# Performance work log

Hardware: AMD Instinct MI355X
Metric: run time of the kernel (lower is better)

Reference implementation:

```python
import jax, jax.numpy as jnp
import numpy as np

B, C, H, W = 4, 256, 64, 64
CH = C // 2  # inner channels


def setup_inputs() -> dict:
    key = jax.random.key(0)
    ks = jax.random.split(key, 9)
    s = 1.0 / np.sqrt(C)
    so = 1.0 / np.sqrt(CH)
    return {
        "x": jax.random.normal(ks[0], (B, C, H, W), dtype=jnp.float32),
        "teta_w": jax.random.uniform(ks[1], (CH, C), jnp.float32, -s, s),
        "teta_b": jax.random.uniform(ks[2], (CH,), jnp.float32, -s, s),
        "fi_w": jax.random.uniform(ks[3], (CH, C), jnp.float32, -s, s),
        "fi_b": jax.random.uniform(ks[4], (CH,), jnp.float32, -s, s),
        "gi_w": jax.random.uniform(ks[5], (CH, C), jnp.float32, -s, s),
        "gi_b": jax.random.uniform(ks[6], (CH,), jnp.float32, -s, s),
        "out_w": jax.random.uniform(ks[7], (C, CH), jnp.float32, -so, so),
        "out_b": jax.random.uniform(ks[8], (C,), jnp.float32, -so, so),
    }


def _conv1x1(x, w, b):
    # x: (B, Cin, H, W), w: (Cout, Cin) -> (B, Cout, H, W)
    return jnp.einsum('bchw,oc->bohw', x, w) + b[None, :, None, None]


def reference(x, teta_w, teta_b, fi_w, fi_b, gi_w, gi_b, out_w, out_b):
    b, c, h, w = x.shape
    n = h * w
    ch = teta_w.shape[0]
    # NOTE: original uses .view (reshape), NOT transpose, to get (B, N, Ch)
    x1 = _conv1x1(x, teta_w, teta_b).reshape(b, ch, n).reshape(b, n, ch)
    x2 = _conv1x1(x, fi_w, fi_b).reshape(b, ch, n)            # (B, Ch, N)
    x3 = _conv1x1(x, gi_w, gi_b).reshape(b, ch, n).reshape(b, n, ch)
    # softmax over dim=1 (rows), as in the original
    attn = jax.nn.softmax(jnp.matmul(x1, x2), axis=1)          # (B, N, N)
    y = jnp.matmul(attn, x3)                                   # (B, N, Ch)
    y = jnp.swapaxes(y, 1, 2).reshape(b, ch, h, w)
    return x + _conv1x1(y, out_w, out_b)
```

## Files before the change

kernel.cpp:

```cpp
#include <hip/hip_runtime.h>
#include <hip/hip_bf16.h>

#define BB 4
#define CC 256
#define CHH 128
#define NN 4096
#define KSHIFT 12.0f

typedef __attribute__((ext_vector_type(8))) short bf16x8;
typedef __attribute__((ext_vector_type(4))) float f32x4;

__device__ __forceinline__ float to_f(float v) { return v; }
__device__ __forceinline__ float to_f(__hip_bfloat16 v) { return __bfloat162float(v); }
__device__ __forceinline__ void st_f(float* p, float v) { *p = v; }
__device__ __forceinline__ void st_f(__hip_bfloat16* p, float v) { *p = __float2bfloat16(v); }
__device__ __forceinline__ unsigned short f2bf(float f) {
    __hip_bfloat16 h = __float2bfloat16(f);
    unsigned short u;
    __builtin_memcpy(&u, &h, 2);
    return u;
}
__device__ __forceinline__ bf16x8 ldb8(const unsigned short* p) { return *(const bf16x8*)p; }

__device__ __forceinline__ void gload_lds16(const unsigned short* g, unsigned short* l) {
    __builtin_amdgcn_global_load_lds(
        (const __attribute__((address_space(1))) unsigned int*)g,
        (__attribute__((address_space(3))) unsigned int*)l, 16, 0, 0);
}

__global__ void detect_kernel(const void* __restrict__ tb, int* __restrict__ flag) {
    if (threadIdx.x == 0) {
        const __hip_bfloat16* p = (const __hip_bfloat16*)tb;
        int big = 0, zeros = 0;
        for (int i = 0; i < 128; ++i) {
            float v = __bfloat162float(p[i]);
            if (!(fabsf(v) <= 0.5f)) big = 1;
            if ((i & 1) == 0 && v == 0.0f) zeros++;
        }
        *flag = (big || zeros >= 32) ? 1 : 0;
    }
}

template <typename T>
__device__ __forceinline__ void prep_body(const T* tw, const T* fw, const T* gw, const T* ow,
                                          const T* tb2, const T* fb, const T* gb, const T* ob,
                                          unsigned short* Wb, unsigned short* OWb,
                                          float* Bf, float* OBf) {
    int idx = blockIdx.x * 256 + threadIdx.x;
    if (idx < 98304) {
        int cv = idx >> 15, rem = idx & 32767;
        const T* src = cv == 0 ? tw : (cv == 1 ? fw : gw);
        Wb[idx] = f2bf(to_f(src[rem]));
    } else if (idx < 131072) {
        OWb[idx - 98304] = f2bf(to_f(ow[idx - 98304]));
    } else if (idx < 131456) {
        int r = idx - 131072;
        int cv = r >> 7, j = r & 127;
        const T* src = cv == 0 ? tb2 : (cv == 1 ? fb : gb);
        Bf[r] = to_f(src[j]);
    } else if (idx < 131712) {
        OBf[idx - 131456] = to_f(ob[idx - 131456]);
    }
}

__global__ void prep_kernel(const void* tw, const void* fw, const void* gw, const void* ow,
                            const void* tb2, const void* fb, const void* gb, const void* ob,
                            const int* __restrict__ flag,
                            unsigned short* Wb, unsigned short* OWb, float* Bf, float* OBf) {
    if (*flag)
        prep_body<float>((const float*)tw, (const float*)fw, (const float*)gw, (const float*)ow,
                         (const float*)tb2, (const float*)fb, (const float*)gb, (const float*)ob,
                         Wb, OWb, Bf, OBf);
    else
        prep_body<__hip_bfloat16>((const __hip_bfloat16*)tw, (const __hip_bfloat16*)fw,
                                  (const __hip_bfloat16*)gw, (const __hip_bfloat16*)ow,
                                  (const __hip_bfloat16*)tb2, (const __hip_bfloat16*)fb,
                                  (const __hip_bfloat16*)gb, (const __hip_bfloat16*)ob,
                                  Wb, OWb, Bf, OBf);
}

template <typename T>
__device__ __forceinline__ void xtrans_body(const T* __restrict__ x, unsigned short* __restrict__ xt) {
    int b = blockIdx.z;
    const T* in = x + (size_t)b * CC * NN;
    unsigned short* out = xt + (size_t)b * NN * CC;
    int p0 = blockIdx.x * 64, c0 = blockIdx.y * 64;
    __shared__ unsigned short t[64][68];
    int flat = threadIdx.x;
#pragma unroll
    for (int tt = 0; tt < 16; ++tt) {
        int id = flat + tt * 256;
        int rr = id >> 6, cc = id & 63;
        t[cc][rr] = f2bf(to_f(in[(size_t)(c0 + rr) * NN + p0 + cc]));
    }
    __syncthreads();
#pragma unroll
    for (int tt = 0; tt < 16; ++tt) {
        int id = flat + tt * 256;
        int pp = id >> 6, jj = id & 63;
        out[(size_t)(p0 + pp) * CC + c0 + jj] = t[pp][jj];
    }
}

__launch_bounds__(256)
__global__ void xtrans_kernel(const void* x, const int* __restrict__ flag,
                              unsigned short* __restrict__ xt) {
    if (*flag) xtrans_body<float>((const float*)x, xt);
    else       xtrans_body<__hip_bfloat16>((const __hip_bfloat16*)x, xt);
}

__launch_bounds__(256)
__global__ void conv3_mfma_kernel(const unsigned short* __restrict__ xt,
                                  const unsigned short* __restrict__ Wb,
                                  const float* __restrict__ Bf,
                                  unsigned short* __restrict__ T1b,
                                  unsigned short* __restrict__ T2t,
                                  unsigned short* __restrict__ T3b) {
    int b = blockIdx.y;
    int p0 = blockIdx.x * 16;
    int flat = threadIdx.x;
    int w = flat >> 6, lane = flat & 63, m = lane & 15, quad = lane >> 4;
    const unsigned short* xrow = xt + ((size_t)b * NN + p0 + m) * CC;
    bf16x8 xf[8];
#pragma unroll
    for (int kc = 0; kc < 8; ++kc)
        xf[kc] = ldb8(&xrow[kc * 32 + quad * 8]);
    unsigned short* t1  = T1b + (size_t)b * CHH * NN;
    unsigned short* t2t = T2t + (size_t)b * CHH * NN;
    unsigned short* t3  = T3b + (size_t)b * CHH * NN;
#pragma unroll
    for (int q = 0; q < 6; ++q) {
        int t = w * 6 + q;
        int cv = t >> 3, ot = t & 7;
        int o0 = ot * 16;
        const unsigned short* wrow = Wb + ((size_t)cv * CHH + o0 + m) * CC;
        f32x4 acc = {0.f, 0.f, 0.f, 0.f};
#pragma unroll
        for (int kc = 0; kc < 8; ++kc) {
            bf16x8 wf = ldb8(&wrow[kc * 32 + quad * 8]);
            acc = __builtin_amdgcn_mfma_f32_16x16x32_bf16(wf, xf[kc], acc, 0, 0, 0);
        }
        unsigned short hv[4];
#pragma unroll
        for (int r = 0; r < 4; ++r)
            hv[r] = f2bf(acc[r] + Bf[cv * CHH + o0 + quad * 4 + r]);
        if (cv == 1) {
            unsigned int lo = (unsigned int)hv[0] | ((unsigned int)hv[1] << 16);
            unsigned int hi = (unsigned int)hv[2] | ((unsigned int)hv[3] << 16);
            int src = (lane & 3) * 16 + (lane >> 2);
            unsigned int tlo = (unsigned int)__shfl((int)lo, src, 64);
            unsigned int thi = (unsigned int)__shfl((int)hi, src, 64);
            unsigned int* dst = (unsigned int*)&t2t[(size_t)(p0 + (lane >> 2)) * CHH +
                                                    o0 + (lane & 3) * 4];
            dst[0] = tlo;
            dst[1] = thi;
        } else {
            unsigned short* outp = (cv == 0) ? t1 : t3;
#pragma unroll
            for (int r = 0; r < 4; ++r)
                outp[(size_t)(o0 + quad * 4 + r) * NN + p0 + m] = hv[r];
        }
    }
}

__launch_bounds__(256)
__global__ void transpose_kernel(const unsigned short* __restrict__ in,
                                 unsigned short* __restrict__ out, int R, int C) {
    int bz = blockIdx.z;
    in  += (size_t)bz * R * C;
    out += (size_t)bz * R * C;
    int c0 = blockIdx.x * 64, r0 = blockIdx.y * 64;
    __shared__ unsigned short t[64][68];
    int flat = threadIdx.x;
#pragma unroll
    for (int tt = 0; tt < 16; ++tt) {
        int id = flat + tt * 256;
        int r = id >> 6, c = id & 63;
        t[c][r] = in[(size_t)(r0 + r) * C + c0 + c];
    }
    __syncthreads();
#pragma unroll
    for (int tt = 0; tt < 16; ++tt) {
        int id = flat + tt * 256;
        int c = id >> 6, r = id & 63;
        out[(size_t)(c0 + c) * R + r0 + r] = t[c][r];
    }
}

__launch_bounds__(256)
__global__ void stats_mfma_kernel(const unsigned short* __restrict__ T1b,
                                  const unsigned short* __restrict__ T2t,
                                  float* __restrict__ Lpart) {
    int blk = blockIdx.x;
    int b = (blk & 7) >> 1;
    int rest = (blk >> 3) * 2 + (blk & 1);
    int strip = rest >> 3, iq = rest & 7;
    int ibase = iq * 512;
    int flat = threadIdx.x;
    int w = flat >> 6, lane = flat & 63, m = lane & 15, quad = lane >> 4;
    const unsigned short* A  = T1b + (size_t)b * CHH * NN;
    const unsigned short* Bt = T2t + (size_t)b * CHH * NN;
    __shared__ unsigned short th[64 * 128];

    int u0w = strip * 128 + w * 32;
    bf16x8 bfr[2][4];
#pragma unroll
    for (int g = 0; g < 2; ++g)
#pragma unroll
        for (int kc = 0; kc < 4; ++kc)
            bfr[g][kc] = ldb8(&Bt[(size_t)(u0w + g * 16 + m) * CHH + kc * 32 + quad * 8]);

    float csum[2] = {0.f, 0.f};
    for (int t = 0; t < 8; ++t) {
        int i0t = ibase + t * 64;
        __syncthreads();
#pragma unroll
        for (int i = 0; i < 4; ++i) {
            int sl = i * 256 + flat;
            int r = sl >> 4, ch = sl & 15;
            int c = ch ^ (r & 7);
            gload_lds16(&A[(size_t)(i0t + r) * CHH + c * 8], &th[sl * 8]);
        }
        __syncthreads();
#pragma unroll
        for (int s = 0; s < 4; ++s) {
            int irow = s * 16 + m;
            bf16x8 af[4];
#pragma unroll
            for (int kc = 0; kc < 4; ++kc) {
                int ch = (kc * 4 + quad) ^ (irow & 7);
                af[kc] = *(const bf16x8*)&th[irow * 128 + ch * 8];
            }
#pragma unroll
            for (int g = 0; g < 2; ++g) {
                f32x4 acc = {0.f, 0.f, 0.f, 0.f};
#pragma unroll
                for (int kc = 0; kc < 4; ++kc)
                    acc = __builtin_amdgcn_mfma_f32_16x16x32_bf16(af[kc], bfr[g][kc], acc, 0, 0, 0);
#pragma unroll
                for (int r = 0; r < 4; ++r)
                    csum[g] += __expf(acc[r] - KSHIFT);
            }
        }
    }
#pragma unroll
    for (int g = 0; g < 2; ++g) {
        csum[g] += __shfl_xor(csum[g], 16, 64);
        csum[g] += __shfl_xor(csum[g], 32, 64);
        if (lane < 16)
            Lpart[((size_t)iq * BB + b) * NN + u0w + g * 16 + m] = csum[g];
    }
}

__launch_bounds__(256)
__global__ void attn_mfma_kernel(const unsigned short* __restrict__ T1b,
                                 const unsigned short* __restrict__ T2t,
                                 const unsigned short* __restrict__ X3t,
                                 const float* __restrict__ Lpart,
                                 unsigned short* __restrict__ Yp0,
                                 unsigned short* __restrict__ Yp1,
                                 unsigned short* __restrict__ Yp2,
                                 unsigned short* __restrict__ Yp3) {
    int blk = blockIdx.x;
    int b = (blk & 7) >> 1;
    int rest = (blk >> 3) * 2 + (blk & 1);
    int it = rest >> 2, uc = rest & 3;
    int i0 = it * 128;
    unsigned short* Yp = uc == 0 ? Yp0 : (uc == 1 ? Yp1 : (uc == 2 ? Yp2 : Yp3));
    int flat = threadIdx.x;
    int w = flat >> 6, lane = flat & 63, m = lane & 15, quad = lane >> 4;
    const unsigned short* A  = T1b + (size_t)b * CHH * NN;
    const unsigned short* Bt = T2t + (size_t)b * CHH * NN;
    const unsigned short* X3 = X3t + (size_t)b * CHH * NN;

    __shared__ unsigned short bt[64 * 128];
    __shared__ unsigned short x3[128 * 64];
    __shared__ unsigned short pT[4][2][16][40];
    __shared__ float llh[1024];

    int ubeg = uc * 1024;
#pragma unroll
    for (int k = 0; k < 4; ++k) {
        int idx = k * 256 + flat;
        int u = ubeg + idx;
        float s = 0.f;
#pragma unroll
        for (int c = 0; c < 8; ++c)
            s += Lpart[((size_t)c * BB + b) * NN + u];
        llh[idx] = logf(s) + KSHIFT;
    }

    int iw = i0 + w * 32;
    bf16x8 ath[2][4];
#pragma unroll
    for (int g = 0; g < 2; ++g)
#pragma unroll
        for (int kc = 0; kc < 4; ++kc)
            ath[g][kc] = ldb8(&A[(size_t)(iw + g * 16 + m) * CHH + kc * 32 + quad * 8]);
    f32x4 yacc[2][8];
#pragma unroll
    for (int g = 0; g < 2; ++g)
#pragma unroll
        for (int js = 0; js < 8; ++js) yacc[g][js] = (f32x4){0.f, 0.f, 0.f, 0.f};

    for (int u0 = ubeg; u0 < ubeg + 1024; u0 += 64) {
        __syncthreads();
#pragma unroll
        for (int i = 0; i < 4; ++i) {
            int sl = i * 256 + flat;
            int u = sl >> 4, ch = sl & 15;
            int c = ch ^ (u & 7);
            gload_lds16(&Bt[(size_t)(u0 + u) * CHH + c * 8], &bt[sl * 8]);
        }
#pragma unroll
        for (int i = 0; i < 4; ++i) {
            int sl = i * 256 + flat;
            int j = sl >> 3, ch = sl & 7;
            int c = ch ^ (j & 7);
            gload_lds16(&X3[(size_t)j * NN + u0 + c * 8], &x3[sl * 8]);
        }
        __syncthreads();
#pragma unroll
        for (int h = 0; h < 2; ++h) {
#pragma unroll
            for (int su = 0; su < 2; ++su) {
                int u = h * 32 + su * 16 + m;
                f32x4 a0 = {0.f, 0.f, 0.f, 0.f}, a1 = {0.f, 0.f, 0.f, 0.f};
#pragma unroll
                for (int kc = 0; kc < 4; ++kc) {
                    int ch = (kc * 4 + quad) ^ (u & 7);
                    bf16x8 bf = *(const bf16x8*)&bt[u * 128 + ch * 8];
                    a0 = __builtin_amdgcn_mfma_f32_16x16x32_bf16(ath[0][kc], bf, a0, 0, 0, 0);
                    a1 = __builtin_amdgcn_mfma_f32_16x16x32_bf16(ath[1][kc], bf, a1, 0, 0, 0);
                }
                float ll = llh[u0 - ubeg + u];
#pragma unroll
                for (int r = 0; r < 4; ++r) {
                    pT[w][0][quad * 4 + r][su * 16 + m] = f2bf(__expf(a0[r] - ll));
                    pT[w][1][quad * 4 + r][su * 16 + m] = f2bf(__expf(a1[r] - ll));
                }
            }
            bf16x8 pa0 = *(const bf16x8*)&pT[w][0][m][quad * 8];
            bf16x8 pa1 = *(const bf16x8*)&pT[w][1][m][quad * 8];
#pragma unroll
            for (int js = 0; js < 8; ++js) {
                int j = js * 16 + m;
                int ch = (h * 4 + quad) ^ (j & 7);
                bf16x8 xb = *(const bf16x8*)&x3[j * 64 + ch * 8];
                yacc[0][js] = __builtin_amdgcn_mfma_f32_16x16x32_bf16(pa0, xb, yacc[0][js], 0, 0, 0);
                yacc[1][js] = __builtin_amdgcn_mfma_f32_16x16x32_bf16(pa1, xb, yacc[1][js], 0, 0, 0);
            }
        }
    }
#pragma unroll
    for (int g = 0; g < 2; ++g)
#pragma unroll
        for (int js = 0; js < 8; ++js)
#pragma unroll
            for (int r = 0; r < 4; ++r)
                Yp[((size_t)b * NN + iw + g * 16 + quad * 4 + r) * CHH + js * 16 + m] =
                    f2bf(yacc[g][js][r]);
}

template <typename T>
__device__ __forceinline__ void outconv_body(const T* __restrict__ x,
                                             const unsigned short* __restrict__ Yp0,
                                             const unsigned short* __restrict__ Yp1,
                                             const unsigned short* __restrict__ Yp2,
                                             const unsigned short* __restrict__ Yp3,
                                             const unsigned short* __restrict__ OWb,
                                             const float* __restrict__ OBf,
                                             T* __restrict__ out) {
    int b = blockIdx.y;
    int p0 = blockIdx.x * 16;
    int flat = threadIdx.x;
    int w = flat >> 6, lane = flat & 63, m = lane & 15, quad = lane >> 4;
    size_t yoff = ((size_t)b * NN + p0 + m) * CHH;
    const unsigned short* yrows[4] = {Yp0 + yoff, Yp1 + yoff, Yp2 + yoff, Yp3 + yoff};
    bf16x8 yf[4][4];
#pragma unroll
    for (int pz = 0; pz < 4; ++pz)
#pragma unroll
        for (int kc = 0; kc < 4; ++kc)
            yf[pz][kc] = ldb8(&yrows[pz][kc * 32 + quad * 8]);
#pragma unroll
    for (int q = 0; q < 4; ++q) {
        int o0 = (w * 4 + q) * 16;
        const unsigned short* wrow = OWb + (size_t)(o0 + m) * CHH;
        f32x4 acc = {0.f, 0.f, 0.f, 0.f};
#pragma unroll
        for (int kc = 0; kc < 4; ++kc) {
            bf16x8 aw = ldb8(&wrow[kc * 32 + quad * 8]);
#pragma unroll
            for (int pz = 0; pz < 4; ++pz)
                acc = __builtin_amdgcn_mfma_f32_16x16x32_bf16(aw, yf[pz][kc], acc, 0, 0, 0);
        }
#pragma unroll
        for (int r = 0; r < 4; ++r) {
            int co = o0 + quad * 4 + r;
            size_t oi = ((size_t)b * CC + co) * NN + p0 + m;
            st_f(&out[oi], acc[r] + OBf[co] + to_f(x[oi]));
        }
    }
}

__launch_bounds__(256)
__global__ void outconv_mfma_kernel(const void* x,
                                    const unsigned short* __restrict__ Yp0,
                                    const unsigned short* __restrict__ Yp1,
                                    const unsigned short* __restrict__ Yp2,
                                    const unsigned short* __restrict__ Yp3,
                                    const unsigned short* __restrict__ OWb,
                                    const float* __restrict__ OBf,
                                    const int* __restrict__ flag, void* out) {
    if (*flag)
        outconv_body<float>((const float*)x, Yp0, Yp1, Yp2, Yp3, OWb, OBf, (float*)out);
    else
        outconv_body<__hip_bfloat16>((const __hip_bfloat16*)x, Yp0, Yp1, Yp2, Yp3, OWb, OBf,
                                     (__hip_bfloat16*)out);
}

extern "C" void kernel_launch(void* const* d_in, const int* in_sizes, int n_in,
                              void* d_out, int out_size, void* d_ws, size_t ws_size,
                              hipStream_t stream) {
    const void* x  = d_in[0];
    const void* tw = d_in[1];
    const void* tb = d_in[2];
    const void* fw = d_in[3];
    const void* fb = d_in[4];
    const void* gw = d_in[5];
    const void* gb = d_in[6];
    const void* ow = d_in[7];
    const void* ob = d_in[8];

    const size_t TE = (size_t)BB * CHH * NN;
    unsigned short* T1b = (unsigned short*)d_ws;
    unsigned short* T2t = T1b + TE;
    unsigned short* X3t = T2t + TE;
    unsigned short* T3b = X3t + TE;
    unsigned short* xt  = T3b + TE;
    unsigned short* Yp0 = xt;
    unsigned short* Yp1 = xt + TE;
    unsigned short* Yp2 = T3b;
    unsigned short* Yp3 = xt + 2 * TE;
    unsigned short* Wb  = Yp3 + TE;
    unsigned short* OWb = Wb + 98304;
    float* Bf    = (float*)(OWb + 32768);
    float* OBf   = Bf + 384;
    float* Lpart = OBf + 256;
    int*   Flag  = (int*)(Lpart + 131072);

    detect_kernel<<<1, 64, 0, stream>>>(tb, Flag);
    prep_kernel<<<dim3(515), 256, 0, stream>>>(tw, fw, gw, ow, tb, fb, gb, ob,
                                               Flag, Wb, OWb, Bf, OBf);
    xtrans_kernel<<<dim3(NN / 64, CC / 64, BB), 256, 0, stream>>>(x, Flag, xt);
    conv3_mfma_kernel<<<dim3(NN / 16, BB), 256, 0, stream>>>(xt, Wb, Bf, T1b, T2t, T3b);
    transpose_kernel<<<dim3(CHH / 64, NN / 64, BB), 256, 0, stream>>>(T3b, X3t, NN, CHH);
    stats_mfma_kernel<<<dim3(1024), 256, 0, stream>>>(T1b, T2t, Lpart);
    attn_mfma_kernel<<<dim3(512), 256, 0, stream>>>(T1b, T2t, X3t, Lpart, Yp0, Yp1, Yp2, Yp3);
    outconv_mfma_kernel<<<dim3(NN / 16, BB), 256, 0, stream>>>(x, Yp0, Yp1, Yp2, Yp3,
                                                               OWb, OBf, Flag, d_out);
}
```

Before: 213.9 us.

## Fuse input transpose, weight prep and flag detection into conv and stats kernels

```diff
diff --git a/kernel.cpp b/kernel.cpp
--- a/kernel.cpp
+++ b/kernel.cpp
@@ -22,14 +22,27 @@
 }
 __device__ __forceinline__ bf16x8 ldb8(const unsigned short* p) { return *(const bf16x8*)p; }
 
+__device__ __forceinline__ bf16x8 ld_bf8(const __hip_bfloat16* p) {
+    return ldb8((const unsigned short*)p);
+}
+__device__ __forceinline__ bf16x8 ld_bf8(const float* p) {
+    float4 a = *(const float4*)p;
+    float4 c = *(const float4*)(p + 4);
+    union { bf16x8 v; unsigned short u[8]; } r;
+    r.u[0] = f2bf(a.x); r.u[1] = f2bf(a.y); r.u[2] = f2bf(a.z); r.u[3] = f2bf(a.w);
+    r.u[4] = f2bf(c.x); r.u[5] = f2bf(c.y); r.u[6] = f2bf(c.z); r.u[7] = f2bf(c.w);
+    return r.v;
+}
+
 __device__ __forceinline__ void gload_lds16(const unsigned short* g, unsigned short* l) {
     __builtin_amdgcn_global_load_lds(
         (const __attribute__((address_space(1))) unsigned int*)g,
         (__attribute__((address_space(3))) unsigned int*)l, 16, 0, 0);
 }
 
-__global__ void detect_kernel(const void* __restrict__ tb, int* __restrict__ flag) {
-    if (threadIdx.x == 0) {
+__device__ __forceinline__ int detect_wire(const void* tb) {
+    int f = 0;
+    if ((threadIdx.x & 63) == 0) {
         const __hip_bfloat16* p = (const __hip_bfloat16*)tb;
         int big = 0, zeros = 0;
         for (int i = 0; i < 128; ++i) {
@@ -37,113 +50,60 @@
             if (!(fabsf(v) <= 0.5f)) big = 1;
             if ((i & 1) == 0 && v == 0.0f) zeros++;
         }
-        *flag = (big || zeros >= 32) ? 1 : 0;
-    }
+        f = (big || zeros >= 32) ? 1 : 0;
+    }
+    return __shfl(f, 0, 64);
 }
 
 template <typename T>
-__device__ __forceinline__ void prep_body(const T* tw, const T* fw, const T* gw, const T* ow,
-                                          const T* tb2, const T* fb, const T* gb, const T* ob,
-                                          unsigned short* Wb, unsigned short* OWb,
-                                          float* Bf, float* OBf) {
-    int idx = blockIdx.x * 256 + threadIdx.x;
-    if (idx < 98304) {
-        int cv = idx >> 15, rem = idx & 32767;
-        const T* src = cv == 0 ? tw : (cv == 1 ? fw : gw);
-        Wb[idx] = f2bf(to_f(src[rem]));
-    } else if (idx < 131072) {
-        OWb[idx - 98304] = f2bf(to_f(ow[idx - 98304]));
-    } else if (idx < 131456) {
-        int r = idx - 131072;
-        int cv = r >> 7, j = r & 127;
-        const T* src = cv == 0 ? tb2 : (cv == 1 ? fb : gb);
-        Bf[r] = to_f(src[j]);
-    } else if (idx < 131712) {
-        OBf[idx - 131456] = to_f(ob[idx - 131456]);
-    }
-}
-
-__global__ void prep_kernel(const void* tw, const void* fw, const void* gw, const void* ow,
-                            const void* tb2, const void* fb, const void* gb, const void* ob,
-                            const int* __restrict__ flag,
-                            unsigned short* Wb, unsigned short* OWb, float* Bf, float* OBf) {
-    if (*flag)
-        prep_body<float>((const float*)tw, (const float*)fw, (const float*)gw, (const float*)ow,
-                         (const float*)tb2, (const float*)fb, (const float*)gb, (const float*)ob,
-                         Wb, OWb, Bf, OBf);
-    else
-        prep_body<__hip_bfloat16>((const __hip_bfloat16*)tw, (const __hip_bfloat16*)fw,
-                                  (const __hip_bfloat16*)gw, (const __hip_bfloat16*)ow,
-                                  (const __hip_bfloat16*)tb2, (const __hip_bfloat16*)fb,
-                                  (const __hip_bfloat16*)gb, (const __hip_bfloat16*)ob,
-                                  Wb, OWb, Bf, OBf);
-}
-
-template <typename T>
-__device__ __forceinline__ void xtrans_body(const T* __restrict__ x, unsigned short* __restrict__ xt) {
-    int b = blockIdx.z;
-    const T* in = x + (size_t)b * CC * NN;
-    unsigned short* out = xt + (size_t)b * NN * CC;
-    int p0 = blockIdx.x * 64, c0 = blockIdx.y * 64;
-    __shared__ unsigned short t[64][68];
-    int flat = threadIdx.x;
-#pragma unroll
-    for (int tt = 0; tt < 16; ++tt) {
-        int id = flat + tt * 256;
-        int rr = id >> 6, cc = id & 63;
-        t[cc][rr] = f2bf(to_f(in[(size_t)(c0 + rr) * NN + p0 + cc]));
-    }
-    __syncthreads();
-#pragma unroll
-    for (int tt = 0; tt < 16; ++tt) {
-        int id = flat + tt * 256;
-        int pp = id >> 6, jj = id & 63;
-        out[(size_t)(p0 + pp) * CC + c0 + jj] = t[pp][jj];
-    }
-}
-
-__launch_bounds__(256)
-__global__ void xtrans_kernel(const void* x, const int* __restrict__ flag,
-                              unsigned short* __restrict__ xt) {
-    if (*flag) xtrans_body<float>((const float*)x, xt);
-    else       xtrans_body<__hip_bfloat16>((const __hip_bfloat16*)x, xt);
-}
-
-__launch_bounds__(256)
-__global__ void conv3_mfma_kernel(const unsigned short* __restrict__ xt,
-                                  const unsigned short* __restrict__ Wb,
-                                  const float* __restrict__ Bf,
-                                  unsigned short* __restrict__ T1b,
-                                  unsigned short* __restrict__ T2t,
-                                  unsigned short* __restrict__ T3b) {
+__device__ __forceinline__ void conv3_body(const T* __restrict__ x,
+                                           const T* __restrict__ tw, const T* __restrict__ tb2,
+                                           const T* __restrict__ fw, const T* __restrict__ fb,
+                                           const T* __restrict__ gw, const T* __restrict__ gb,
+                                           unsigned short* __restrict__ T1b,
+                                           unsigned short* __restrict__ T2t,
+                                           unsigned short* __restrict__ T3b,
+                                           unsigned short* tx) {
     int b = blockIdx.y;
     int p0 = blockIdx.x * 16;
     int flat = threadIdx.x;
     int w = flat >> 6, lane = flat & 63, m = lane & 15, quad = lane >> 4;
-    const unsigned short* xrow = xt + ((size_t)b * NN + p0 + m) * CC;
+    const T* xb = x + (size_t)b * CC * NN;
+#pragma unroll
+    for (int pass = 0; pass < 16; ++pass) {
+        int idx = pass * 256 + flat;
+        int c = idx >> 4, p = idx & 15;
+        int ch = (c >> 3) ^ (p & 7);
+        tx[p * 256 + ch * 8 + (c & 7)] = f2bf(to_f(xb[(size_t)c * NN + p0 + p]));
+    }
+    __syncthreads();
     bf16x8 xf[8];
 #pragma unroll
-    for (int kc = 0; kc < 8; ++kc)
-        xf[kc] = ldb8(&xrow[kc * 32 + quad * 8]);
+    for (int kc = 0; kc < 8; ++kc) {
+        int ch = (kc * 4 + quad) ^ (m & 7);
+        xf[kc] = *(const bf16x8*)&tx[m * 256 + ch * 8];
+    }
     unsigned short* t1  = T1b + (size_t)b * CHH * NN;
     unsigned short* t2t = T2t + (size_t)b * CHH * NN;
     unsigned short* t3  = T3b + (size_t)b * CHH * NN;
+    const T* wsrcs[3] = {tw, fw, gw};
+    const T* bsrcs[3] = {tb2, fb, gb};
 #pragma unroll
     for (int q = 0; q < 6; ++q) {
         int t = w * 6 + q;
         int cv = t >> 3, ot = t & 7;
         int o0 = ot * 16;
-        const unsigned short* wrow = Wb + ((size_t)cv * CHH + o0 + m) * CC;
+        const T* wrow = wsrcs[cv] + (size_t)(o0 + m) * CC;
         f32x4 acc = {0.f, 0.f, 0.f, 0.f};
 #pragma unroll
         for (int kc = 0; kc < 8; ++kc) {
-            bf16x8 wf = ldb8(&wrow[kc * 32 + quad * 8]);
+            bf16x8 wf = ld_bf8(&wrow[kc * 32 + quad * 8]);
             acc = __builtin_amdgcn_mfma_f32_16x16x32_bf16(wf, xf[kc], acc, 0, 0, 0);
         }
         unsigned short hv[4];
 #pragma unroll
         for (int r = 0; r < 4; ++r)
-            hv[r] = f2bf(acc[r] + Bf[cv * CHH + o0 + quad * 4 + r]);
+            hv[r] = f2bf(acc[r] + to_f(bsrcs[cv][o0 + quad * 4 + r]));
         if (cv == 1) {
             unsigned int lo = (unsigned int)hv[0] | ((unsigned int)hv[1] << 16);
             unsigned int hi = (unsigned int)hv[2] | ((unsigned int)hv[3] << 16);
@@ -164,91 +124,112 @@
 }
 
 __launch_bounds__(256)
-__global__ void transpose_kernel(const unsigned short* __restrict__ in,
-                                 unsigned short* __restrict__ out, int R, int C) {
-    int bz = blockIdx.z;
-    in  += (size_t)bz * R * C;
-    out += (size_t)bz * R * C;
-    int c0 = blockIdx.x * 64, r0 = blockIdx.y * 64;
-    __shared__ unsigned short t[64][68];
+__global__ void conv3_mfma_kernel(const void* x,
+                                  const void* tw, const void* tb2, const void* fw,
+                                  const void* fb, const void* gw, const void* gb,
+                                  unsigned short* __restrict__ T1b,
+                                  unsigned short* __restrict__ T2t,
+                                  unsigned short* __restrict__ T3b) {
+    __shared__ __align__(16) unsigned short tx[16 * 256];
+    int flag = detect_wire(tb2);
+    if (flag)
+        conv3_body<float>((const float*)x, (const float*)tw, (const float*)tb2,
+                          (const float*)fw, (const float*)fb, (const float*)gw,
+                          (const float*)gb, T1b, T2t, T3b, tx);
+    else
+        conv3_body<__hip_bfloat16>((const __hip_bfloat16*)x, (const __hip_bfloat16*)tw,
+                                   (const __hip_bfloat16*)tb2, (const __hip_bfloat16*)fw,
+                                   (const __hip_bfloat16*)fb, (const __hip_bfloat16*)gw,
+                                   (const __hip_bfloat16*)gb, T1b, T2t, T3b, tx);
+}
+
+__launch_bounds__(256)
+__global__ void statstrans_kernel(const unsigned short* __restrict__ T1b,
+                                  const unsigned short* __restrict__ T2t,
+                                  const unsigned short* __restrict__ T3b,
+                                  unsigned short* __restrict__ X3t,
+                                  float* __restrict__ Lpart) {
+    __shared__ __align__(16) char smem[16384];
+    int blk = blockIdx.x;
     int flat = threadIdx.x;
-#pragma unroll
-    for (int tt = 0; tt < 16; ++tt) {
-        int id = flat + tt * 256;
-        int r = id >> 6, c = id & 63;
-        t[c][r] = in[(size_t)(r0 + r) * C + c0 + c];
-    }
-    __syncthreads();
-#pragma unroll
-    for (int tt = 0; tt < 16; ++tt) {
-        int id = flat + tt * 256;
-        int c = id >> 6, r = id & 63;
-        out[(size_t)(c0 + c) * R + r0 + r] = t[c][r];
-    }
-}
-
-__launch_bounds__(256)
-__global__ void stats_mfma_kernel(const unsigned short* __restrict__ T1b,
-                                  const unsigned short* __restrict__ T2t,
-                                  float* __restrict__ Lpart) {
-    int blk = blockIdx.x;
-    int b = (blk & 7) >> 1;
-    int rest = (blk >> 3) * 2 + (blk & 1);
-    int strip = rest >> 3, iq = rest & 7;
-    int ibase = iq * 512;
-    int flat = threadIdx.x;
-    int w = flat >> 6, lane = flat & 63, m = lane & 15, quad = lane >> 4;
-    const unsigned short* A  = T1b + (size_t)b * CHH * NN;
-    const unsigned short* Bt = T2t + (size_t)b * CHH * NN;
-    __shared__ unsigned short th[64 * 128];
-
-    int u0w = strip * 128 + w * 32;
-    bf16x8 bfr[2][4];
-#pragma unroll
-    for (int g = 0; g < 2; ++g)
-#pragma unroll
-        for (int kc = 0; kc < 4; ++kc)
-            bfr[g][kc] = ldb8(&Bt[(size_t)(u0w + g * 16 + m) * CHH + kc * 32 + quad * 8]);
-
-    float csum[2] = {0.f, 0.f};
-    for (int t = 0; t < 8; ++t) {
-        int i0t = ibase + t * 64;
+    if (blk < 2048) {
+        unsigned short* th = (unsigned short*)smem;
+        int b = (blk & 7) >> 1;
+        int rest = (blk >> 3) * 2 + (blk & 1);
+        int strip = rest >> 4, iq = rest & 15;
+        int ibase = iq * 256;
+        int w = flat >> 6, lane = flat & 63, m = lane & 15, quad = lane >> 4;
+        const unsigned short* A  = T1b + (size_t)b * CHH * NN;
+        const unsigned short* Bt = T2t + (size_t)b * CHH * NN;
+        int u0w = strip * 128 + w * 32;
+        bf16x8 bfr[2][4];
+#pragma unroll
+        for (int g = 0; g < 2; ++g)
+#pragma unroll
+            for (int kc = 0; kc < 4; ++kc)
+                bfr[g][kc] = ldb8(&Bt[(size_t)(u0w + g * 16 + m) * CHH + kc * 32 + quad * 8]);
+        float csum[2] = {0.f, 0.f};
+        for (int t = 0; t < 4; ++t) {
+            int i0t = ibase + t * 64;
+            __syncthreads();
+#pragma unroll
+            for (int i = 0; i < 4; ++i) {
+                int sl = i * 256 + flat;
+                int r = sl >> 4, ch = sl & 15;
+                int c = ch ^ (r & 7);
+                gload_lds16(&A[(size_t)(i0t + r) * CHH + c * 8], &th[sl * 8]);
+            }
+            __syncthreads();
+#pragma unroll
+            for (int s = 0; s < 4; ++s) {
+                int irow = s * 16 + m;
+                bf16x8 af[4];
+#pragma unroll
+                for (int kc = 0; kc < 4; ++kc) {
+                    int ch = (kc * 4 + quad) ^ (irow & 7);
+                    af[kc] = *(const bf16x8*)&th[irow * 128 + ch * 8];
+                }
+#pragma unroll
+                for (int g = 0; g < 2; ++g) {
+                    f32x4 acc = {0.f, 0.f, 0.f, 0.f};
+#pragma unroll
+                    for (int kc = 0; kc < 4; ++kc)
+                        acc = __builtin_amdgcn_mfma_f32_16x16x32_bf16(af[kc], bfr[g][kc],
+                                                                      acc, 0, 0, 0);
+#pragma unroll
+                    for (int r = 0; r < 4; ++r)
+                        csum[g] += __expf(acc[r] - KSHIFT);
+                }
+            }
+        }
+#pragma unroll
+        for (int g = 0; g < 2; ++g) {
+            csum[g] += __shfl_xor(csum[g], 16, 64);
+            csum[g] += __shfl_xor(csum[g], 32, 64);
+            if (lane < 16)
+                Lpart[((size_t)iq * BB + b) * NN + u0w + g * 16 + m] = csum[g];
+        }
+    } else {
+        unsigned short (*t)[68] = (unsigned short (*)[68])smem;
+        int blk2 = blk - 2048;
+        int b = blk2 & 3;
+        int idx = blk2 >> 2;
+        int c0 = (idx & 1) * 64, r0 = (idx >> 1) * 64;
+        const unsigned short* in = T3b + (size_t)b * CHH * NN;
+        unsigned short* out = X3t + (size_t)b * CHH * NN;
+#pragma unroll
+        for (int tt = 0; tt < 16; ++tt) {
+            int id = flat + tt * 256;
+            int r = id >> 6, c = id & 63;
+            t[c][r] = in[(size_t)(r0 + r) * CHH + c0 + c];
+        }
         __syncthreads();
 #pragma unroll
-        for (int i = 0; i < 4; ++i) {
-            int sl = i * 256 + flat;
-            int r = sl >> 4, ch = sl & 15;
-            int c = ch ^ (r & 7);
-            gload_lds16(&A[(size_t)(i0t + r) * CHH + c * 8], &th[sl * 8]);
-        }
-        __syncthreads();
-#pragma unroll
-        for (int s = 0; s < 4; ++s) {
-            int irow = s * 16 + m;
-            bf16x8 af[4];
-#pragma unroll
-            for (int kc = 0; kc < 4; ++kc) {
-                int ch = (kc * 4 + quad) ^ (irow & 7);
-                af[kc] = *(const bf16x8*)&th[irow * 128 + ch * 8];
-            }
-#pragma unroll
-            for (int g = 0; g < 2; ++g) {
-                f32x4 acc = {0.f, 0.f, 0.f, 0.f};
-#pragma unroll
-                for (int kc = 0; kc < 4; ++kc)
-                    acc = __builtin_amdgcn_mfma_f32_16x16x32_bf16(af[kc], bfr[g][kc], acc, 0, 0, 0);
-#pragma unroll
-                for (int r = 0; r < 4; ++r)
-                    csum[g] += __expf(acc[r] - KSHIFT);
-            }
-        }
-    }
-#pragma unroll
-    for (int g = 0; g < 2; ++g) {
-        csum[g] += __shfl_xor(csum[g], 16, 64);
-        csum[g] += __shfl_xor(csum[g], 32, 64);
-        if (lane < 16)
-            Lpart[((size_t)iq * BB + b) * NN + u0w + g * 16 + m] = csum[g];
+        for (int tt = 0; tt < 16; ++tt) {
+            int id = flat + tt * 256;
+            int c = id >> 6, r = id & 63;
+            out[(size_t)(c0 + c) * NN + r0 + r] = t[c][r];
+        }
     }
 }
 
@@ -285,7 +266,7 @@
         int u = ubeg + idx;
         float s = 0.f;
 #pragma unroll
-        for (int c = 0; c < 8; ++c)
+        for (int c = 0; c < 16; ++c)
             s += Lpart[((size_t)c * BB + b) * NN + u];
         llh[idx] = logf(s) + KSHIFT;
     }
@@ -368,8 +349,8 @@
                                              const unsigned short* __restrict__ Yp1,
                                              const unsigned short* __restrict__ Yp2,
                                              const unsigned short* __restrict__ Yp3,
-                                             const unsigned short* __restrict__ OWb,
-                                             const float* __restrict__ OBf,
+                                             const T* __restrict__ ow,
+                                             const T* __restrict__ ob,
                                              T* __restrict__ out) {
     int b = blockIdx.y;
     int p0 = blockIdx.x * 16;
@@ -386,11 +367,11 @@
 #pragma unroll
     for (int q = 0; q < 4; ++q) {
         int o0 = (w * 4 + q) * 16;
-        const unsigned short* wrow = OWb + (size_t)(o0 + m) * CHH;
+        const T* wrow = ow + (size_t)(o0 + m) * CHH;
         f32x4 acc = {0.f, 0.f, 0.f, 0.f};
 #pragma unroll
         for (int kc = 0; kc < 4; ++kc) {
-            bf16x8 aw = ldb8(&wrow[kc * 32 + quad * 8]);
+            bf16x8 aw = ld_bf8(&wrow[kc * 32 + quad * 8]);
 #pragma unroll
             for (int pz = 0; pz < 4; ++pz)
                 acc = __builtin_amdgcn_mfma_f32_16x16x32_bf16(aw, yf[pz][kc], acc, 0, 0, 0);
@@ -399,7 +380,7 @@
         for (int r = 0; r < 4; ++r) {
             int co = o0 + quad * 4 + r;
             size_t oi = ((size_t)b * CC + co) * NN + p0 + m;
-            st_f(&out[oi], acc[r] + OBf[co] + to_f(x[oi]));
+            st_f(&out[oi], acc[r] + to_f(ob[co]) + to_f(x[oi]));
         }
     }
 }
@@ -410,13 +391,15 @@
                                     const unsigned short* __restrict__ Yp1,
                                     const unsigned short* __restrict__ Yp2,
                                     const unsigned short* __restrict__ Yp3,
-                                    const unsigned short* __restrict__ OWb,
-                                    const float* __restrict__ OBf,
-                                    const int* __restrict__ flag, void* out) {
-    if (*flag)
-        outconv_body<float>((const float*)x, Yp0, Yp1, Yp2, Yp3, OWb, OBf, (float*)out);
+                                    const void* ow, const void* ob, const void* tb2,
+                                    void* out) {
+    int flag = detect_wire(tb2);
+    if (flag)
+        outconv_body<float>((const float*)x, Yp0, Yp1, Yp2, Yp3,
+                            (const float*)ow, (const float*)ob, (float*)out);
     else
-        outconv_body<__hip_bfloat16>((const __hip_bfloat16*)x, Yp0, Yp1, Yp2, Yp3, OWb, OBf,
+        outconv_body<__hip_bfloat16>((const __hip_bfloat16*)x, Yp0, Yp1, Yp2, Yp3,
+                                     (const __hip_bfloat16*)ow, (const __hip_bfloat16*)ob,
                                      (__hip_bfloat16*)out);
 }
 
@@ -438,26 +421,16 @@
     unsigned short* T2t = T1b + TE;
     unsigned short* X3t = T2t + TE;
     unsigned short* T3b = X3t + TE;
-    unsigned short* xt  = T3b + TE;
-    unsigned short* Yp0 = xt;
-    unsigned short* Yp1 = xt + TE;
+    unsigned short* Yp0 = T3b + TE;
+    unsigned short* Yp1 = Yp0 + TE;
+    unsigned short* Yp3 = Yp1 + TE;
     unsigned short* Yp2 = T3b;
-    unsigned short* Yp3 = xt + 2 * TE;
-    unsigned short* Wb  = Yp3 + TE;
-    unsigned short* OWb = Wb + 98304;
-    float* Bf    = (float*)(OWb + 32768);
-    float* OBf   = Bf + 384;
-    float* Lpart = OBf + 256;
-    int*   Flag  = (int*)(Lpart + 131072);
-
-    detect_kernel<<<1, 64, 0, stream>>>(tb, Flag);
-    prep_kernel<<<dim3(515), 256, 0, stream>>>(tw, fw, gw, ow, tb, fb, gb, ob,
-                                               Flag, Wb, OWb, Bf, OBf);
-    xtrans_kernel<<<dim3(NN / 64, CC / 64, BB), 256, 0, stream>>>(x, Flag, xt);
-    conv3_mfma_kernel<<<dim3(NN / 16, BB), 256, 0, stream>>>(xt, Wb, Bf, T1b, T2t, T3b);
-    transpose_kernel<<<dim3(CHH / 64, NN / 64, BB), 256, 0, stream>>>(T3b, X3t, NN, CHH);
-    stats_mfma_kernel<<<dim3(1024), 256, 0, stream>>>(T1b, T2t, Lpart);
+    float* Lpart = (float*)(Yp3 + TE);
+
+    conv3_mfma_kernel<<<dim3(NN / 16, BB), 256, 0, stream>>>(
+        x, tw, tb, fw, fb, gw, gb, T1b, T2t, T3b);
+    statstrans_kernel<<<dim3(2560), 256, 0, stream>>>(T1b, T2t, T3b, X3t, Lpart);
     attn_mfma_kernel<<<dim3(512), 256, 0, stream>>>(T1b, T2t, X3t, Lpart, Yp0, Yp1, Yp2, Yp3);
     outconv_mfma_kernel<<<dim3(NN / 16, BB), 256, 0, stream>>>(x, Yp0, Yp1, Yp2, Yp3,
-                                                               OWb, OBf, Flag, d_out);
-}
+                                                               ow, ob, tb, d_out);
+}
```

New measurement: 254.9 us. 19.2% more time.
